# Optimization experiments

Measured on AMD Instinct MI355X. Metric: run time of the kernel, lower is better.

Reference implementation:

```python
import jax, jax.numpy as jnp
import numpy as np

B, C, H, W = 8, 64, 200, 320
N = 48            # bboxes (table rows) per image
STRIDE = 4        # pad_w / W
WD = W // STRIDE  # kernel-branch width after downsampling


def setup_inputs() -> dict:
    key = jax.random.key(0)
    ks = jax.random.split(key, 10)
    feats = jax.random.normal(ks[0], (B, C, H, W), dtype=jnp.float32)
    kernel_feats = jax.random.normal(ks[1], (B, C, H, WD), dtype=jnp.float32)
    Wk = jax.random.normal(ks[2], (C + 1, C), dtype=jnp.float32) * 0.05
    bk = jax.random.normal(ks[3], (C + 1,), dtype=jnp.float32) * 0.05
    Wf = jax.random.normal(ks[4], (C, C), dtype=jnp.float32) * 0.05
    bf = jax.random.normal(ks[5], (C,), dtype=jnp.float32) * 0.05
    # bboxes in padded-image pixels; only y1,y2 matter for line_type='row'.
    yc_idx = jax.random.randint(ks[6], (B, N), 0, H).astype(jnp.float32)
    y1 = yc_idx * STRIDE
    y2 = y1  # center = y coordinate exactly on a feature row
    x1 = jnp.zeros((B, N), jnp.float32)
    x2 = jnp.full((B, N), float(W * STRIDE), jnp.float32)
    det_bboxes = jnp.stack([x1, y1, x2, y2], axis=-1)  # [B,N,4]
    image_shape = jax.random.randint(ks[7], (B, 2), 400, 800).astype(jnp.int32)  # [img_w,img_h]
    return {
        "feats": feats, "kernel_feats": kernel_feats,
        "Wk": Wk, "bk": bk, "Wf": Wf, "bf": bf,
        "det_bboxes": det_bboxes, "image_shape": image_shape, "pad_w": 1280,
    }


def reference(feats, kernel_feats, Wk, bk, Wf, bf, det_bboxes, image_shape, pad_w):
    b, c, h, w = feats.shape
    stride = pad_w / w  # 4.0
    # kernel_conv (1x1) then mean over width (line_type='row')
    kernels = jnp.einsum('oc,bchw->bohw', Wk, kernel_feats) + bk[None, :, None, None]
    kernels = kernels.mean(-1)                         # [B, C+1, H]
    # feats_conv (1x1)
    f = jnp.einsum('oc,bchw->bohw', Wf, feats) + bf[None, :, None, None]
    # valid-region masks from per-image (img_w, img_h)
    hlim = (image_shape[:, 1].astype(jnp.float32) / stride).astype(jnp.int32)
    wlim = (image_shape[:, 0].astype(jnp.float32) / stride).astype(jnp.int32)
    mask = (jnp.arange(h)[None, :, None] < hlim[:, None, None]) & \
           (jnp.arange(w)[None, None, :] < wlim[:, None, None])   # [B,H,W]
    # gather per-bbox dynamic kernels at row centers
    yc = (det_bboxes[..., 1] + det_bboxes[..., 3]) / (2.0 * stride)  # [B,N]
    idx = yc.astype(jnp.int32)
    vk = kernels[jnp.arange(b)[:, None], :, idx]       # [B,N,C+1]
    wgt, bias = vk[..., :c], vk[..., c]
    # grouped 1x1 conv == per-instance matvec over channels
    logits = jnp.einsum('bnc,bchw->bnhw', wgt, f) + bias[..., None, None]
    logits = jnp.where(mask[:, None, :, :], logits, jnp.float32(-1e8))
    centers = (yc * stride)[..., None]                 # [B,N,1]
    return logits, centers
```

## Files before the change

### kernel.cpp

```cpp
#include <hip/hip_runtime.h>

#define Bb 8
#define Cc 64
#define Hh 200
#define Ww 320
#define Nn 48
#define WDd 80
#define HW (Hh*Ww)

__global__ __launch_bounds__(256) void prep_kernel(
    const float* __restrict__ kf, const float* __restrict__ Wk,
    const float* __restrict__ bk, const float* __restrict__ Wf,
    const float* __restrict__ bf, const float* __restrict__ db,
    const int* __restrict__ pad_w,
    float* __restrict__ weffT, float* __restrict__ beff,
    float* __restrict__ centers)
{
    const int n = blockIdx.x, b = blockIdx.y, tid = threadIdx.x;
    const int c = tid & 63, q = tid >> 6;
    const float stride = (float)pad_w[0] / (float)Ww;
    const float yc = (db[(b*Nn + n)*4 + 1] + db[(b*Nn + n)*4 + 3]) / (2.0f * stride);
    const int idx = (int)yc;

    __shared__ float part[Cc][5];
    __shared__ float kfm[Cc];
    __shared__ float vk[Cc + 1];

    {
        const float4* row = (const float4*)(kf + ((size_t)(b*Cc + c)*Hh + idx)*WDd) + q*5;
        float4 v0 = row[0], v1 = row[1], v2 = row[2], v3 = row[3], v4 = row[4];
        float s = (v0.x+v0.y+v0.z+v0.w) + (v1.x+v1.y+v1.z+v1.w)
                + (v2.x+v2.y+v2.z+v2.w) + (v3.x+v3.y+v3.z+v3.w)
                + (v4.x+v4.y+v4.z+v4.w);
        part[c][q] = s;
    }
    __syncthreads();
    if (tid < Cc)
        kfm[tid] = (part[tid][0]+part[tid][1]+part[tid][2]+part[tid][3]) * (1.0f/(float)WDd);
    __syncthreads();

    if (tid < Cc + 1) {
        float a = bk[tid];
        const float4* wr = (const float4*)(Wk + tid*Cc);
        #pragma unroll
        for (int i = 0; i < 16; ++i) {
            float4 wv = wr[i];
            a = fmaf(wv.x, kfm[4*i+0], a);
            a = fmaf(wv.y, kfm[4*i+1], a);
            a = fmaf(wv.z, kfm[4*i+2], a);
            a = fmaf(wv.w, kfm[4*i+3], a);
        }
        vk[tid] = a;
    }
    __syncthreads();

    if (tid < Cc) {
        float wsum = 0.f;
        #pragma unroll 8
        for (int c2 = 0; c2 < Cc; ++c2) wsum = fmaf(vk[c2], Wf[c2*Cc + tid], wsum);
        weffT[((size_t)b*Cc + tid)*Nn + n] = wsum;
    } else if (tid == Cc) {
        float bb2 = vk[Cc];
        #pragma unroll 8
        for (int c2 = 0; c2 < Cc; ++c2) bb2 = fmaf(vk[c2], bf[c2], bb2);
        beff[b*Nn + n] = bb2;
        centers[b*Nn + n] = yc * stride;
    }
}

__global__ __launch_bounds__(64) void logits_kernel(
    const float* __restrict__ feats, const int* __restrict__ ishape,
    const int* __restrict__ pad_w, const float* __restrict__ weffT,
    const float* __restrict__ beff, float* __restrict__ out)
{
    const int b = blockIdx.z;
    const int h = blockIdx.y;
    const int w0 = blockIdx.x * 128 + threadIdx.x * 2;

    const float stride = (float)pad_w[0] / (float)Ww;
    const int hlim = (int)((float)ishape[b*2 + 1] / stride);
    const int wlim = (int)((float)ishape[b*2 + 0] / stride);
    const bool inb  = (w0 < Ww);
    const bool act0 = inb && (h < hlim) && (w0     < wlim);
    const bool act1 = inb && (h < hlim) && (w0 + 1 < wlim);

    float2 acc[Nn];
    if (__ballot(act0 || act1) != 0ULL) {
        const float* __restrict__ bv = beff + b*Nn;
        #pragma unroll
        for (int n = 0; n < Nn; ++n) { acc[n].x = bv[n]; acc[n].y = bv[n]; }

        const float* __restrict__ fp = feats + ((size_t)(b*Cc)*Hh + h)*Ww + (inb ? w0 : 0);
        const float* __restrict__ wT = weffT + (size_t)b*Cc*Nn;
        #pragma unroll 4
        for (int c = 0; c < Cc; ++c) {
            const float2 fv = *(const float2*)(fp + (size_t)c * HW);
            const float* __restrict__ wrow = wT + c*Nn;
            #pragma unroll
            for (int n = 0; n < Nn; ++n) {
                acc[n].x = fmaf(wrow[n], fv.x, acc[n].x);
                acc[n].y = fmaf(wrow[n], fv.y, acc[n].y);
            }
        }
    } else {
        #pragma unroll
        for (int n = 0; n < Nn; ++n) { acc[n].x = -1e8f; acc[n].y = -1e8f; }
    }

    if (inb) {
        float* op = out + ((size_t)(b*Nn)*Hh + h)*Ww + w0;
        #pragma unroll
        for (int n = 0; n < Nn; ++n) {
            float2 v;
            v.x = act0 ? acc[n].x : -1e8f;
            v.y = act1 ? acc[n].y : -1e8f;
            *(float2*)(op + (size_t)n * HW) = v;
        }
    }
}

extern "C" void kernel_launch(void* const* d_in, const int* in_sizes, int n_in,
                              void* d_out, int out_size, void* d_ws, size_t ws_size,
                              hipStream_t stream) {
    const float* feats  = (const float*)d_in[0];
    const float* kf     = (const float*)d_in[1];
    const float* Wk     = (const float*)d_in[2];
    const float* bk     = (const float*)d_in[3];
    const float* Wf     = (const float*)d_in[4];
    const float* bf     = (const float*)d_in[5];
    const float* db     = (const float*)d_in[6];
    const int*   ishape = (const int*)d_in[7];
    const int*   pad_w  = (const int*)d_in[8];

    float* out    = (float*)d_out;
    float* weffT  = (float*)d_ws;
    float* beff   = weffT + (size_t)Bb*Cc*Nn;
    float* centers = out + (size_t)Bb*Nn*Hh*Ww;

    prep_kernel<<<dim3(Nn, Bb), 256, 0, stream>>>(
        kf, Wk, bk, Wf, bf, db, pad_w, weffT, beff, centers);

    logits_kernel<<<dim3((Ww + 127)/128, Hh, Bb), 64, 0, stream>>>(
        feats, ishape, pad_w, weffT, beff, out);
}
```

Measured before the change: 250.3 us.

## Flatten logits grid to 256-thread blocks and use nontemporal loads/stores

After: 254.4 us. About the same (+1.7%).

```diff
diff --git a/kernel.cpp b/kernel.cpp
--- a/kernel.cpp
+++ b/kernel.cpp
@@ -7,6 +7,9 @@
 #define Nn 48
 #define WDd 80
 #define HW (Hh*Ww)
+#define U2 (HW/2)
+
+typedef float vfloat2 __attribute__((ext_vector_type(2)));
 
 __global__ __launch_bounds__(256) void prep_kernel(
     const float* __restrict__ kf, const float* __restrict__ Wk,
@@ -68,55 +71,55 @@
     }
 }
 
-__global__ __launch_bounds__(64) void logits_kernel(
+__global__ __launch_bounds__(256) void logits_kernel(
     const float* __restrict__ feats, const int* __restrict__ ishape,
     const int* __restrict__ pad_w, const float* __restrict__ weffT,
     const float* __restrict__ beff, float* __restrict__ out)
 {
-    const int b = blockIdx.z;
-    const int h = blockIdx.y;
-    const int w0 = blockIdx.x * 128 + threadIdx.x * 2;
+    const int b = blockIdx.y;
+    const int u = blockIdx.x * 256 + threadIdx.x;
+    const int h  = u / (Ww/2);
+    const int w0 = (u - h*(Ww/2)) * 2;
 
     const float stride = (float)pad_w[0] / (float)Ww;
     const int hlim = (int)((float)ishape[b*2 + 1] / stride);
     const int wlim = (int)((float)ishape[b*2 + 0] / stride);
-    const bool inb  = (w0 < Ww);
-    const bool act0 = inb && (h < hlim) && (w0     < wlim);
-    const bool act1 = inb && (h < hlim) && (w0 + 1 < wlim);
+    const bool act0 = (h < hlim) && (w0     < wlim);
+    const bool act1 = (h < hlim) && (w0 + 1 < wlim);
 
-    float2 acc[Nn];
-    if (__ballot(act0 || act1) != 0ULL) {
+    vfloat2 acc[Nn];
+    if (__ballot(act0) != 0ULL) {
         const float* __restrict__ bv = beff + b*Nn;
         #pragma unroll
-        for (int n = 0; n < Nn; ++n) { acc[n].x = bv[n]; acc[n].y = bv[n]; }
+        for (int n = 0; n < Nn; ++n) { acc[n][0] = bv[n]; acc[n][1] = bv[n]; }
 
-        const float* __restrict__ fp = feats + ((size_t)(b*Cc)*Hh + h)*Ww + (inb ? w0 : 0);
+        const float* __restrict__ fp = feats + (size_t)b*Cc*HW + 2*u;
         const float* __restrict__ wT = weffT + (size_t)b*Cc*Nn;
         #pragma unroll 4
         for (int c = 0; c < Cc; ++c) {
-            const float2 fv = *(const float2*)(fp + (size_t)c * HW);
+            const vfloat2 fv = __builtin_nontemporal_load(
+                (const vfloat2*)(fp + (size_t)c * HW));
             const float* __restrict__ wrow = wT + c*Nn;
             #pragma unroll
             for (int n = 0; n < Nn; ++n) {
-                acc[n].x = fmaf(wrow[n], fv.x, acc[n].x);
-                acc[n].y = fmaf(wrow[n], fv.y, acc[n].y);
+                acc[n][0] = fmaf(wrow[n], fv[0], acc[n][0]);
+                acc[n][1] = fmaf(wrow[n], fv[1], acc[n][1]);
             }
+        }
+        #pragma unroll
+        for (int n = 0; n < Nn; ++n) {
+            acc[n][0] = act0 ? acc[n][0] : -1e8f;
+            acc[n][1] = act1 ? acc[n][1] : -1e8f;
         }
     } else {
         #pragma unroll
-        for (int n = 0; n < Nn; ++n) { acc[n].x = -1e8f; acc[n].y = -1e8f; }
+        for (int n = 0; n < Nn; ++n) { acc[n][0] = -1e8f; acc[n][1] = -1e8f; }
     }
 
-    if (inb) {
-        float* op = out + ((size_t)(b*Nn)*Hh + h)*Ww + w0;
-        #pragma unroll
-        for (int n = 0; n < Nn; ++n) {
-            float2 v;
-            v.x = act0 ? acc[n].x : -1e8f;
-            v.y = act1 ? acc[n].y : -1e8f;
-            *(float2*)(op + (size_t)n * HW) = v;
-        }
-    }
+    float* op = out + (size_t)b*Nn*HW + 2*u;
+    #pragma unroll
+    for (int n = 0; n < Nn; ++n)
+        __builtin_nontemporal_store(acc[n], (vfloat2*)(op + (size_t)n * HW));
 }
 
 extern "C" void kernel_launch(void* const* d_in, const int* in_sizes, int n_in,
@@ -140,6 +143,6 @@
     prep_kernel<<<dim3(Nn, Bb), 256, 0, stream>>>(
         kf, Wk, bk, Wf, bf, db, pad_w, weffT, beff, centers);
 
-    logits_kernel<<<dim3((Ww + 127)/128, Hh, Bb), 64, 0, stream>>>(
+    logits_kernel<<<dim3(U2/256, Bb), 256, 0, stream>>>(
         feats, ishape, pad_w, weffT, beff, out);
 }
```
